# Performance work log

Measured on AMD Instinct MI355X. Metric: run time of the kernel, lower is better.

## Reference

```python
import jax, jax.numpy as jnp
import numpy as np

EPS = 1e-6
LOSS_WEIGHT = 1.0


def _sigma_components(xywhr):
    """Closed-form symmetric 2x2 covariance Sigma = R diag((w/2)^2,(h/2)^2) R^T.
    Returns the three independent components (s00, s01, s11)."""
    wh = jnp.clip(xywhr[..., 2:4], 1e-7, 1e7)
    r = xywhr[..., 4]
    c, s = jnp.cos(r), jnp.sin(r)
    a = (0.5 * wh[..., 0]) ** 2  # (w/2)^2
    b = (0.5 * wh[..., 1]) ** 2  # (h/2)^2
    s00 = a * c * c + b * s * s
    s01 = (a - b) * s * c
    s11 = a * s * s + b * c * c
    return s00, s01, s11


def setup_inputs() -> dict:
    key = jax.random.key(0)
    kp, kt = jax.random.split(key)
    pred = jax.random.uniform(kp, (4096, 5), dtype=jnp.float32)
    target = jax.random.uniform(kt, (2048, 5), dtype=jnp.float32)
    return {"pred": pred, "target": target}


def reference(pred, target):
    # box_decode is identity here (boxes already xywhr). match=True path -> (M, N) cost.
    p00, p01, p11 = _sigma_components(pred)    # each (M,)
    t00, t01, t11 = _sigma_components(target)  # each (N,)

    det_p = p00 * p11 - p01 * p01
    det_t = t00 * t11 - t01 * t01
    Vb_p = 4.0 * jnp.sqrt(jnp.abs(det_p))[:, None]  # (M, 1)
    Vb_t = 4.0 * jnp.sqrt(jnp.abs(det_t))[None, :]  # (1, N)

    # Broadcast pred components over columns, target over rows -> (M, N) planes.
    p00, p01, p11 = p00[:, None], p01[:, None], p11[:, None]
    t00, t01, t11 = t00[None, :], t01[None, :], t11[None, :]

    # Sum S = Sigma_p + Sigma_t (symmetric), closed-form 2x2 inverse.
    m00, m01, m11 = p00 + t00, p01 + t01, p11 + t11
    det_m = m00 * m11 - m01 * m01
    i00, i01, i11 = m11 / det_m, -m01 / det_m, m00 / det_m

    # K = Sigma_p @ inv(S)  (generally non-symmetric)
    k00 = p00 * i00 + p01 * i01
    k01 = p00 * i01 + p01 * i11
    k10 = p01 * i00 + p11 * i01
    k11 = p01 * i01 + p11 * i11

    # Sigma = Sigma_p - K @ Sigma_p
    sig00 = p00 - (k00 * p00 + k01 * p01)
    sig01 = p01 - (k00 * p01 + k01 * p11)
    sig10 = p01 - (k10 * p00 + k11 * p01)
    sig11 = p11 - (k10 * p01 + k11 * p11)
    det_sig = sig00 * sig11 - sig01 * sig10

    Vb = 4.0 * jnp.sqrt(jnp.abs(det_sig))  # (M, N)
    KFIoU = Vb / (Vb_p + Vb_t - Vb + EPS)
    # fun='none': loss = 1 - KFIoU, clamped at 0; reduction='none'
    loss = jnp.clip(1.0 - KFIoU, 0.0)
    return loss * LOSS_WEIGHT
```

## Files before the change

### kernel.cpp

```cpp
#include <hip/hip_runtime.h>
#include <cmath>


typedef float v2f __attribute__((ext_vector_type(2)));

constexpr int ROWS  = 16;
constexpr int BCOLS = 512;

__device__ __forceinline__ void sincos_cr(float rf, float* sf, float* cf) {
  double x = (double)rf;
  if (fabs(x) <= 1.0) {
    double z = x * x;
    double ps = -7.647163731819816e-13;
    ps = fma(ps, z, 1.605904383682161e-10);
    ps = fma(ps, z, -2.505210838544172e-08);
    ps = fma(ps, z, 2.755731922398589e-06);
    ps = fma(ps, z, -1.984126984126984e-04);
    ps = fma(ps, z, 8.333333333333333e-03);
    ps = fma(ps, z, -1.666666666666667e-01);
    double s = fma(ps * z, x, x);
    double pc = 1.561920696858623e-16;
    pc = fma(pc, z, -4.779477332387385e-14);
    pc = fma(pc, z, 1.147074559772972e-11);
    pc = fma(pc, z, -2.087675698786810e-09);
    pc = fma(pc, z, 2.755731922398589e-07);
    pc = fma(pc, z, -2.480158730158730e-05);
    pc = fma(pc, z, 1.388888888888889e-03);
    pc = fma(pc, z, -4.166666666666666e-02);
    pc = fma(pc, z, 5.000000000000000e-01);
    double c = fma(-pc, z, 1.0);
    *sf = (float)s;
    *cf = (float)c;
  } else {
    *sf = sinf(rf);
    *cf = cosf(rf);
  }
}

__device__ __forceinline__ float4 box_params(const float* __restrict__ bx) {
#pragma clang fp contract(off)
  float w = fminf(fmaxf(bx[2], 1e-7f), 1e7f);
  float h = fminf(fmaxf(bx[3], 1e-7f), 1e7f);
  float s, c;
  sincos_cr(bx[4], &s, &c);
  float a = (0.5f * w) * (0.5f * w);
  float b = (0.5f * h) * (0.5f * h);
  float s00 = a * c * c + b * s * s;
  float s01 = (a - b) * s * c;
  float s11 = a * s * s + b * c * c;
  float det = s00 * s11 - s01 * s01;
  float vb  = 4.0f * __fsqrt_rn(fabsf(det));
  return make_float4(s00, s01, s11, vb);
}

__device__ __forceinline__ v2f rcp_refined(v2f d) {
  v2f r;
  r[0] = __builtin_amdgcn_rcpf(d[0]);
  r[1] = __builtin_amdgcn_rcpf(d[1]);
  v2f one = {1.0f, 1.0f};
  v2f e = __builtin_elementwise_fma(-d, r, one);
  return __builtin_elementwise_fma(e, r, r);
}
__device__ __forceinline__ v2f div_faithful(v2f a, v2f d, v2f r) {
  v2f q = a * r;
  v2f e = __builtin_elementwise_fma(-d, q, a);
  return __builtin_elementwise_fma(e, r, q);
}

__device__ __forceinline__ v2f kf_chain(v2f px, v2f py, v2f pz, v2f pw,
                                        float4 t) {
#pragma clang fp contract(off)
  v2f m00 = px + t.x;
  v2f m01 = py + t.y;
  v2f m11 = pz + t.z;
  v2f det_m = m00 * m11 - m01 * m01;

  v2f r = rcp_refined(det_m);
  v2f i00 = div_faithful(m11, det_m, r);
  v2f i01 = div_faithful(-m01, det_m, r);
  v2f i11 = div_faithful(m00, det_m, r);

  v2f k00 = px * i00 + py * i01;
  v2f k01 = px * i01 + py * i11;
  v2f k10 = py * i00 + pz * i01;
  v2f k11 = py * i01 + pz * i11;

  v2f sig00 = px - (k00 * px + k01 * py);
  v2f sig01 = py - (k00 * py + k01 * pz);
  v2f sig10 = py - (k10 * px + k11 * py);
  v2f sig11 = pz - (k10 * py + k11 * pz);

  v2f det_sig = sig00 * sig11 - sig01 * sig10;
  v2f vb;
  vb[0] = 4.0f * __builtin_amdgcn_sqrtf(fabsf(det_sig[0]));
  vb[1] = 4.0f * __builtin_amdgcn_sqrtf(fabsf(det_sig[1]));

  v2f denom = pw + t.w - vb + 1e-6f;
  v2f kf;
  kf[0] = vb[0] * __builtin_amdgcn_rcpf(denom[0]);
  kf[1] = vb[1] * __builtin_amdgcn_rcpf(denom[1]);

  v2f one = {1.0f, 1.0f};
  v2f res = one - kf;
  res[0] = fmaxf(res[0], 0.0f);
  res[1] = fmaxf(res[1], 0.0f);
  return res;
}

__global__ __launch_bounds__(256, 4) void kf_loss_fused(
    const float* __restrict__ pred, const float* __restrict__ target,
    float* __restrict__ out, int nt) {
  __shared__ float4 sp[ROWS];

  const int tid  = threadIdx.x;
  const int row0 = blockIdx.x * ROWS;
  const int col0 = blockIdx.y * BCOLS;

  if (tid < ROWS) sp[tid] = box_params(pred + (size_t)(row0 + tid) * 5);
  const int colA = col0 + tid;
  const int colB = colA + 256;
  const float4 tA = box_params(target + (size_t)colA * 5);
  const float4 tB = box_params(target + (size_t)colB * 5);
  __syncthreads();

  float* oA = out + (size_t)row0 * (size_t)nt + (size_t)colA;
  float* oB = oA + (size_t)nt;

  #pragma unroll
  for (int rr = 0; rr < ROWS; rr += 2) {
    float4 p0 = sp[rr];
    float4 p1 = sp[rr + 1];
    v2f px = {p0.x, p1.x};
    v2f py = {p0.y, p1.y};
    v2f pz = {p0.z, p1.z};
    v2f pw = {p0.w, p1.w};

    v2f ra = kf_chain(px, py, pz, pw, tA);
    v2f rb = kf_chain(px, py, pz, pw, tB);

    oA[0]   = ra[0];
    oA[256] = rb[0];
    oB[0]   = ra[1];
    oB[256] = rb[1];
    oA += (size_t)2 * (size_t)nt;
    oB += (size_t)2 * (size_t)nt;
  }
}

__global__ __launch_bounds__(256) void box_param_kernel(
    const float* __restrict__ pred, int np,
    const float* __restrict__ target, int nt,
    float4* __restrict__ ws) {
  int i = blockIdx.x * 256 + threadIdx.x;
  int n = np + nt;
  if (i >= n) return;
  const float* bx = (i < np) ? (pred + (size_t)i * 5)
                             : (target + (size_t)(i - np) * 5);
  ws[i] = box_params(bx);
}

__device__ __forceinline__ float rcp_ref_s(float d) {
  float r = __builtin_amdgcn_rcpf(d);
  return fmaf(fmaf(-d, r, 1.0f), r, r);
}
__device__ __forceinline__ float div_f_s(float a, float d, float r) {
  float q = a * r;
  return fmaf(fmaf(-d, q, a), r, q);
}
__device__ float kf_pair_s(float4 p, float4 t) {
#pragma clang fp contract(off)
  float m00 = p.x + t.x, m01 = p.y + t.y, m11 = p.z + t.z;
  float det_m = m00 * m11 - m01 * m01;
  float r = rcp_ref_s(det_m);
  float i00 = div_f_s(m11, det_m, r);
  float i01 = div_f_s(-m01, det_m, r);
  float i11 = div_f_s(m00, det_m, r);
  float k00 = p.x * i00 + p.y * i01;
  float k01 = p.x * i01 + p.y * i11;
  float k10 = p.y * i00 + p.z * i01;
  float k11 = p.y * i01 + p.z * i11;
  float sig00 = p.x - (k00 * p.x + k01 * p.y);
  float sig01 = p.y - (k00 * p.y + k01 * p.z);
  float sig10 = p.y - (k10 * p.x + k11 * p.y);
  float sig11 = p.z - (k10 * p.y + k11 * p.z);
  float det_sig = sig00 * sig11 - sig01 * sig10;
  float vb = 4.0f * __builtin_amdgcn_sqrtf(fabsf(det_sig));
  float denom = p.w + t.w - vb + 1e-6f;
  return fmaxf(1.0f - vb * __builtin_amdgcn_rcpf(denom), 0.0f);
}

__global__ __launch_bounds__(256) void kf_loss_edge(
    const float4* __restrict__ pp, const float4* __restrict__ tp,
    float* __restrict__ out, int np, int nt) {
  const int col  = blockIdx.y * 256 + threadIdx.x;
  const int row0 = blockIdx.x * ROWS;
  if (col >= nt) return;
  const float4 t = tp[col];
  int rend = ROWS;
  if (row0 + rend > np) rend = np - row0;
  float* o = out + (size_t)row0 * (size_t)nt + col;
  for (int rr = 0; rr < rend; ++rr) {
    *o = kf_pair_s(pp[row0 + rr], t);
    o += nt;
  }
}

extern "C" void kernel_launch(void* const* d_in, const int* in_sizes, int n_in,
                              void* d_out, int out_size, void* d_ws, size_t ws_size,
                              hipStream_t stream) {
  const float* pred   = (const float*)d_in[0];
  const float* target = (const float*)d_in[1];
  float* out = (float*)d_out;
  int np = in_sizes[0] / 5;
  int nt = in_sizes[1] / 5;

  if ((np % ROWS) == 0 && (nt % BCOLS) == 0) {
    dim3 grid(np / ROWS, nt / BCOLS);
    kf_loss_fused<<<grid, dim3(256), 0, stream>>>(pred, target, out, nt);
  } else {
    float4* params = (float4*)d_ws;
    int nbox = np + nt;
    box_param_kernel<<<(nbox + 255) / 256, 256, 0, stream>>>(
        pred, np, target, nt, params);
    dim3 grid((np + ROWS - 1) / ROWS, (nt + 255) / 256);
    kf_loss_edge<<<grid, dim3(256), 0, stream>>>(
        params, params + np, out, np, nt);
  }
}
```

Baseline: 19.51 us.

## Give each thread four contiguous target columns and store results as float4

Each thread now owns four adjacent target columns instead of two columns 256 apart, and the block covers 1024 columns. Every row's results are written with a single 16-byte vector store, and the packed v2f lanes now span target pairs instead of pred row pairs. The aim is fewer, wider global store instructions on a write-bound output. In exchange each thread computes box parameters for four targets, there are half as many blocks in y, and the loop is only partially unrolled.

```diff
diff --git a/kernel.cpp b/kernel.cpp
--- a/kernel.cpp
+++ b/kernel.cpp
@@ -5,7 +5,8 @@
 typedef float v2f __attribute__((ext_vector_type(2)));
 
 constexpr int ROWS  = 16;
-constexpr int BCOLS = 512;
+constexpr int TCOLS = 4;
+constexpr int BCOLS = 1024;
 
 __device__ __forceinline__ void sincos_cr(float rf, float* sf, float* cf) {
   double x = (double)rf;
@@ -67,12 +68,12 @@
   return __builtin_elementwise_fma(e, r, q);
 }
 
-__device__ __forceinline__ v2f kf_chain(v2f px, v2f py, v2f pz, v2f pw,
-                                        float4 t) {
+__device__ __forceinline__ v2f kf_chain(float4 p, v2f tx, v2f ty, v2f tz,
+                                        v2f tw) {
 #pragma clang fp contract(off)
-  v2f m00 = px + t.x;
-  v2f m01 = py + t.y;
-  v2f m11 = pz + t.z;
+  v2f m00 = tx + p.x;
+  v2f m01 = ty + p.y;
+  v2f m11 = tz + p.z;
   v2f det_m = m00 * m11 - m01 * m01;
 
   v2f r = rcp_refined(det_m);
@@ -80,22 +81,22 @@
   v2f i01 = div_faithful(-m01, det_m, r);
   v2f i11 = div_faithful(m00, det_m, r);
 
-  v2f k00 = px * i00 + py * i01;
-  v2f k01 = px * i01 + py * i11;
-  v2f k10 = py * i00 + pz * i01;
-  v2f k11 = py * i01 + pz * i11;
-
-  v2f sig00 = px - (k00 * px + k01 * py);
-  v2f sig01 = py - (k00 * py + k01 * pz);
-  v2f sig10 = py - (k10 * px + k11 * py);
-  v2f sig11 = pz - (k10 * py + k11 * pz);
+  v2f k00 = p.x * i00 + p.y * i01;
+  v2f k01 = p.x * i01 + p.y * i11;
+  v2f k10 = p.y * i00 + p.z * i01;
+  v2f k11 = p.y * i01 + p.z * i11;
+
+  v2f sig00 = p.x - (k00 * p.x + k01 * p.y);
+  v2f sig01 = p.y - (k00 * p.y + k01 * p.z);
+  v2f sig10 = p.y - (k10 * p.x + k11 * p.y);
+  v2f sig11 = p.z - (k10 * p.y + k11 * p.z);
 
   v2f det_sig = sig00 * sig11 - sig01 * sig10;
   v2f vb;
   vb[0] = 4.0f * __builtin_amdgcn_sqrtf(fabsf(det_sig[0]));
   vb[1] = 4.0f * __builtin_amdgcn_sqrtf(fabsf(det_sig[1]));
 
-  v2f denom = pw + t.w - vb + 1e-6f;
+  v2f denom = tw + p.w - vb + 1e-6f;
   v2f kf;
   kf[0] = vb[0] * __builtin_amdgcn_rcpf(denom[0]);
   kf[1] = vb[1] * __builtin_amdgcn_rcpf(denom[1]);
@@ -117,33 +118,28 @@
   const int col0 = blockIdx.y * BCOLS;
 
   if (tid < ROWS) sp[tid] = box_params(pred + (size_t)(row0 + tid) * 5);
-  const int colA = col0 + tid;
-  const int colB = colA + 256;
-  const float4 tA = box_params(target + (size_t)colA * 5);
-  const float4 tB = box_params(target + (size_t)colB * 5);
+
+  const int colBase = col0 + tid * TCOLS;
+  float4 t0 = box_params(target + (size_t)(colBase + 0) * 5);
+  float4 t1 = box_params(target + (size_t)(colBase + 1) * 5);
+  float4 t2 = box_params(target + (size_t)(colBase + 2) * 5);
+  float4 t3 = box_params(target + (size_t)(colBase + 3) * 5);
+  v2f txA = {t0.x, t1.x}, tyA = {t0.y, t1.y}, tzA = {t0.z, t1.z},
+      twA = {t0.w, t1.w};
+  v2f txB = {t2.x, t3.x}, tyB = {t2.y, t3.y}, tzB = {t2.z, t3.z},
+      twB = {t2.w, t3.w};
   __syncthreads();
 
-  float* oA = out + (size_t)row0 * (size_t)nt + (size_t)colA;
-  float* oB = oA + (size_t)nt;
-
-  #pragma unroll
-  for (int rr = 0; rr < ROWS; rr += 2) {
-    float4 p0 = sp[rr];
-    float4 p1 = sp[rr + 1];
-    v2f px = {p0.x, p1.x};
-    v2f py = {p0.y, p1.y};
-    v2f pz = {p0.z, p1.z};
-    v2f pw = {p0.w, p1.w};
-
-    v2f ra = kf_chain(px, py, pz, pw, tA);
-    v2f rb = kf_chain(px, py, pz, pw, tB);
-
-    oA[0]   = ra[0];
-    oA[256] = rb[0];
-    oB[0]   = ra[1];
-    oB[256] = rb[1];
-    oA += (size_t)2 * (size_t)nt;
-    oB += (size_t)2 * (size_t)nt;
+  float* o = out + (size_t)row0 * (size_t)nt + (size_t)colBase;
+
+  #pragma unroll 4
+  for (int rr = 0; rr < ROWS; ++rr) {
+    float4 p = sp[rr];
+    v2f ra = kf_chain(p, txA, tyA, tzA, twA);
+    v2f rb = kf_chain(p, txB, tyB, tzB, twB);
+    float4 res = make_float4(ra[0], ra[1], rb[0], rb[1]);
+    *reinterpret_cast<float4*>(o) = res;
+    o += (size_t)nt;
   }
 }
 
```

Result: no change. 19.73 us (+1.1%).
